# Kernel tuning notes

Hardware: AMD Instinct MI355X
Metric: run time of the kernel (lower is better)

## Reference

```python
import jax, jax.numpy as jnp
import numpy as np

C = 32           # in_channels
KH, KW = 3, 3    # kernel_range
SHIFT = 1
NP = KH * KW


def conv2d(x, w, b, pad):
    # x: NCHW, w: OIHW
    y = jax.lax.conv_general_dilated(
        x, w, window_strides=(1, 1), padding=[(pad, pad), (pad, pad)],
        dimension_numbers=('NCHW', 'OIHW', 'NCHW'))
    return y + b[None, :, None, None]


def setup_inputs() -> dict:
    key = jax.random.key(0)
    ks = jax.random.split(key, 14)
    p = lambda k, shape: (jax.random.normal(k, shape, dtype=jnp.float32) * 0.02)
    inp = {
        'x':  jax.random.normal(ks[0], (4, C, 256, 256), dtype=jnp.float32),
        'wk': p(ks[1], (C * NP, C, 1, 1)), 'bk': p(ks[2], (C * NP,)),
        'wv': p(ks[3], (C * NP, C, 1, 1)), 'bv': p(ks[4], (C * NP,)),
        'wq': p(ks[5], (C, C, 1, 1)),      'bq': p(ks[6], (C,)),
        'w1': p(ks[7], (C, C, 3, 3)),      'b1': p(ks[8], (C,)),
        'w2': p(ks[9], (2 * C, C, 3, 3)),  'b2': p(ks[10], (2 * C,)),
        'w3': p(ks[11], (C, 2 * C, 3, 3)), 'b3': p(ks[12], (C,)),
    }
    return inp


def reference(x, wk, bk, wv, bv, wq, bq, w1, b1, w2, b2, w3, b3):
    B, D, H, W = x.shape
    h_half, w_half = KH // 2, KW // 2
    ph, pw = h_half * SHIFT, w_half * SHIFT

    x_k = conv2d(x, wk, bk, 0)  # (B, D*NP, H, W)
    x_v = conv2d(x, wv, bv, 0)
    x_q = conv2d(x, wq, bq, 0)  # (B, D, H, W)

    pad4 = ((0, 0), (0, 0), (ph, ph), (pw, pw))
    x_k = jnp.pad(x_k, pad4)
    x_v = jnp.pad(x_v, pad4)
    mask_pad = jnp.pad(jnp.ones((B, 1, H, W), x.dtype), pad4)

    k_ls, v_ls, m_ls = [], [], []
    layer = 0
    for i in range(-h_half, h_half + 1):
        for j in range(-w_half, w_half + 1):
            r0 = ph + i * SHIFT
            c0 = pw + j * SHIFT
            k_ls.append(x_k[:, layer * D:(layer + 1) * D, r0:r0 + H, c0:c0 + W])
            v_ls.append(x_v[:, layer * D:(layer + 1) * D, r0:r0 + H, c0:c0 + W])
            m_ls.append(mask_pad[:, :, r0:r0 + H, c0:c0 + W])
            layer += 1

    # Faithful to torch .view semantics: flat row-major reshape, NOT a permute.
    k = jnp.stack(k_ls, axis=1).reshape(B * H * W, NP, D)   # (B,NP,D,H,W) -> flat
    v = jnp.stack(v_ls, axis=1).reshape(B * H * W, NP, D)
    m = jnp.stack(m_ls, axis=1).reshape(B * H * W, NP, 1)
    q = x_q.reshape(B * H * W, 1, D)                         # (B,D,H,W) -> flat

    scores = jnp.matmul(k, jnp.swapaxes(q, -1, -2)) * m / 8.0  # (N, NP, 1)
    alpha = jax.nn.softmax(scores, axis=1)
    res = jnp.matmul(jnp.swapaxes(alpha, -1, -2), v)           # (N, 1, D)
    t = res.reshape(B, D, H, W)

    t = jax.nn.relu(conv2d(t, w1, b1, 1))
    t = jax.nn.relu(conv2d(t, w2, b2, 1))
    t = jax.nn.relu(conv2d(t, w3, b3, 1))
    return t
```

## Files before the change

kernel.cpp:

```cpp
#include <hip/hip_runtime.h>
#include <hip/hip_bf16.h>

#define B_ 4
#define C_ 32
#define H_ 256
#define W_ 256
#define S_ 65536
#define NP_ 9
#define OC_ 288
#define PR 258
#define PWN 264
#define XGUARD 260
#define XSTRIDE 66056

using bf16 = __hip_bfloat16;
typedef __attribute__((ext_vector_type(8)))  short  short8;
typedef __attribute__((ext_vector_type(4)))  short  short4_t;
typedef __attribute__((ext_vector_type(2)))  short  short2_t;
typedef __attribute__((ext_vector_type(16))) float  f32x16;

__device__ __forceinline__ float b2f(short s) {
    return __uint_as_float(((unsigned)(unsigned short)s) << 16);
}

template<int IC, int OC>
__device__ __forceinline__ void prepA_body(int fid, const float* __restrict__ w,
                                           bf16* __restrict__ apk)
{
    constexpr int NK = 9 * IC / 16;
    int tile = fid >> 9;
    int l = (fid >> 3) & 63;
    int j = fid & 7;
    int mt = tile / NK;
    int ks = tile - mt * NK;
    int q = l >> 5;
    int oc = mt * 32 + (l & 31);
    int k = ks * 16 + q * 8 + j;
    int tap = k / IC;
    int ic = k - tap * IC;
    apk[fid] = __float2bfloat16(w[((oc * IC + ic) * 3 + tap / 3) * 3 + tap % 3]);
}

template<int G>
__device__ __forceinline__ void zerob_body(int b, int p, uint4* __restrict__ buf)
{
    int gran;
    if (p < 2 * PWN * G) {
        int row = (p < PWN * G) ? 0 : 257;
        int rem = p % (PWN * G);
        gran = row * PWN * G + rem;
    } else {
        int p2 = p - 2 * PWN * G;
        int col = (p2 < 256 * G) ? 0 : 257;
        int rem = p2 % (256 * G);
        int r = rem / G + 1;
        int icg = rem - (rem / G) * G;
        gran = (r * PWN + col) * G + icg;
    }
    buf[(size_t)b * PR * PWN * G + gran] = uint4{0, 0, 0, 0};
}

__global__ __launch_bounds__(256) void k_prep(
    const float* __restrict__ wk, const float* __restrict__ wv,
    const float* __restrict__ wq,
    const float* __restrict__ w1, const float* __restrict__ w2,
    const float* __restrict__ w3,
    bf16* __restrict__ apk0, bf16* __restrict__ apk1,
    bf16* __restrict__ apk2, bf16* __restrict__ apk3,
    uint4* __restrict__ tA, uint4* __restrict__ t1, uint4* __restrict__ t2,
    uint4* __restrict__ xb16)
{
    int idx = blockIdx.x * 256 + threadIdx.x;
    if (idx < 19456) {
        int j    = idx & 7;
        int lane = (idx >> 3) & 63;
        int ks   = (idx >> 9) & 1;
        int mt   = idx >> 10;
        int oc = lane & 31;
        int ic = ks * 16 + (lane >> 5) * 8 + j;
        const float* w; int ocg;
        if (mt < 9)       { w = wk; ocg = mt * 32 + oc; }
        else if (mt < 18) { w = wv; ocg = (mt - 9) * 32 + oc; }
        else              { w = wq; ocg = oc; }
        apk0[idx] = __float2bfloat16(w[ocg * C_ + ic]);
    } else if (idx < 28672) {
        prepA_body<32, 32>(idx - 19456, w1, apk1);
    } else if (idx < 47104) {
        prepA_body<32, 64>(idx - 28672, w2, apk2);
    } else if (idx < 65536) {
        prepA_body<64, 32>(idx - 47104, w3, apk3);
    } else if (idx < 82176) {
        int i5 = idx - 65536;
        zerob_body<4>(i5 / 4160, i5 % 4160, tA);
    } else if (idx < 98816) {
        int i6 = idx - 82176;
        zerob_body<4>(i6 / 4160, i6 % 4160, t1);
    } else if (idx < 132096) {
        int i7 = idx - 98816;
        zerob_body<8>(i7 / 8320, i7 % 8320, t2);
    } else if (idx < 142464) {
        int i8 = idx - 132096;
        size_t off;
        if (i8 < 8320) {
            int b = i8 / 2080, r = i8 - b * 2080;
            if (r < 1040) off = (size_t)b * (XSTRIDE * 4) + r;
            else          off = ((size_t)b * XSTRIDE + XGUARD + 65536) * 4 + (r - 1040);
        } else {
            off = (size_t)(4 * XSTRIDE) * 4 + (i8 - 8320);
        }
        xb16[off] = uint4{0, 0, 0, 0};
    }
}

__global__ __launch_bounds__(256) void k_q(
    const float* __restrict__ x, const bf16* __restrict__ apk,
    const float* __restrict__ bq, bf16* __restrict__ xqs, bf16* __restrict__ xb16)
{
    __shared__ bf16 lbuf[32][140];
    int bh  = blockIdx.x >> 9;
    int blk = blockIdx.x & 511;
    int pixw0 = blk << 7;
    int tid  = threadIdx.x;
    int wvi  = tid >> 6;
    int lane = tid & 63;
    int col  = lane & 31, q = lane >> 5;
    int pix  = pixw0 + wvi * 32 + col;

    const float* xb = x + (size_t)bh * (C_ * S_);

    short8 bfrag[2];
#pragma unroll
    for (int kk = 0; kk < 2; ++kk)
#pragma unroll
        for (int j = 0; j < 8; ++j) {
            bf16 h = __float2bfloat16(xb[(size_t)(kk * 16 + q * 8 + j) * S_ + pix]);
            bfrag[kk][j] = *reinterpret_cast<short*>(&h);
        }

    {
        bf16* xr = xb16 + ((size_t)bh * XSTRIDE + XGUARD + pix) * 32;
        *reinterpret_cast<short8*>(xr + (q << 3))       = bfrag[0];
        *reinterpret_cast<short8*>(xr + ((2 + q) << 3)) = bfrag[1];
    }

    const short8* apkv = reinterpret_cast<const short8*>(apk);
    f32x16 acc = {};
    acc = __builtin_amdgcn_mfma_f32_32x32x16_bf16(bfrag[0], apkv[(18 * 2 + 0) * 64 + lane], acc, 0, 0, 0);
    acc = __builtin_amdgcn_mfma_f32_32x32x16_bf16(bfrag[1], apkv[(18 * 2 + 1) * 64 + lane], acc, 0, 0, 0);
    float bbv = bq[col];
#pragma unroll
    for (int g4 = 0; g4 < 4; ++g4) {
        short4_t sv;
#pragma unroll
        for (int j = 0; j < 4; ++j) {
            bf16 hb = __float2bfloat16(acc[g4 * 4 + j] + bbv);
            sv[j] = *reinterpret_cast<short*>(&hb);
        }
        *reinterpret_cast<short4_t*>(&lbuf[col][wvi * 32 + 8 * g4 + 4 * q]) = sv;
    }
    __syncthreads();
    int ch0 = tid >> 4, chk = tid & 15, ch1 = ch0 + 16;
    short8 v0 = *reinterpret_cast<const short8*>(&lbuf[ch0][chk * 8]);
    short8 v1 = *reinterpret_cast<const short8*>(&lbuf[ch1][chk * 8]);
    int tb = (pixw0 >> 5) + (chk >> 2);
    int G2 = chk & 3;
    bf16* qb = xqs + (size_t)bh * (32 * S_);
    short4_t lo0 = {v0[0], v0[1], v0[2], v0[3]}, hi0 = {v0[4], v0[5], v0[6], v0[7]};
    short4_t lo1 = {v1[0], v1[1], v1[2], v1[3]}, hi1 = {v1[4], v1[5], v1[6], v1[7]};
    *reinterpret_cast<short4_t*>(qb + (ch0 * 2048 + tb) * 32 + G2 * 4)      = lo0;
    *reinterpret_cast<short4_t*>(qb + (ch0 * 2048 + tb) * 32 + 16 + G2 * 4) = hi0;
    *reinterpret_cast<short4_t*>(qb + (ch1 * 2048 + tb) * 32 + G2 * 4)      = lo1;
    *reinterpret_cast<short4_t*>(qb + (ch1 * 2048 + tb) * 32 + 16 + G2 * 4) = hi1;
}


#define DO_TILE(T, SQ)                                                                \
{                                                                                     \
    int Tg = tgbase + (T);                                                            \
    if (Tg < 2048) {                                                                  \
        bool hbad = ((((T) << 5) < hb_lo) || (((T) << 5) >= hb_hi));                  \
        if (hbad) {                                                                   \
            if (q == (SQ)) scL[(T) * 32 + col] = 0.f;                                 \
            short4_t z = {0, 0, 0, 0};                                                \
            _Pragma("unroll")                                                         \
            for (int G2 = 0; G2 < 4; ++G2)                                            \
                *reinterpret_cast<short4_t*>(kvB + col * 1616 +                       \
                    ((((T) << 2) + (G2 ^ xcol)) << 4) + q * 8) = z;                   \
        } else {                                                                      \
            unsigned n = (unsigned)plane_base + ((unsigned)Tg << 5);                  \
            unsigned tl = n / 288u;                                                   \
            const bf16* qp = xqb + ((size_t)tl << 5) + (q << 4);                      \
            short8 qA = *reinterpret_cast<const short8*>(qp);                         \
            short8 qB = *reinterpret_cast<const short8*>(qp + 8);                     \
            int xib = ((T) << 5) + 257 + shf + col;                                   \
            int swx = (xib ^ (xib >> 2)) & 3;                                         \
            short8 fa = *reinterpret_cast<const short8*>(&xs[xib * 4 + (q ^ swx)]);   \
            short8 fb = *reinterpret_cast<const short8*>(&xs[xib * 4 + ((2 + q) ^ swx)]); \
            bool tb_lo = (dj == -1) && ((Tg & 7) == 0);                               \
            bool tb_hi = (dj == 1) && ((Tg & 7) == 7);                                \
            if (tb_lo) { if (q == 0) qA[0] = 0; }                                     \
            if (tb_hi) { if (q == 1) qB[7] = 0; }                                     \
            f32x16 ka = {bK, bK, bK, bK, bK, bK, bK, bK, bK, bK, bK, bK, bK, bK, bK, bK}; \
            ka = __builtin_amdgcn_mfma_f32_32x32x16_bf16(fa, apkv[(p * 2 + 0) * 64 + lane], ka, 0, 0, 0); \
            ka = __builtin_amdgcn_mfma_f32_32x32x16_bf16(fb, apkv[(p * 2 + 1) * 64 + lane], ka, 0, 0, 0); \
            float dot = 0.f;                                                          \
            _Pragma("unroll")                                                         \
            for (int j3 = 0; j3 < 4; ++j3) {                                          \
                dot += ka[j3]      * b2f(qA[j3]);                                     \
                dot += ka[4 + j3]  * b2f(qA[4 + j3]);                                 \
                dot += ka[8 + j3]  * b2f(qB[j3]);                                     \
                dot += ka[12 + j3] * b2f(qB[4 + j3]);                                 \
            }                                                                         \
            dot += __shfl_xor(dot, 32);                                               \
            if (q == (SQ)) scL[(T) * 32 + col] = dot;                                 \
            f32x16 vh = {bV, bV, bV, bV, bV, bV, bV, bV, bV, bV, bV, bV, bV, bV, bV, bV}; \
            vh = __builtin_amdgcn_mfma_f32_32x32x16_bf16(fa, apkv[((9 + p) * 2 + 0) * 64 + lane], vh, 0, 0, 0); \
            vh = __builtin_amdgcn_mfma_f32_32x32x16_bf16(fb, apkv[((9 + p) * 2 + 1) * 64 + lane], vh, 0, 0, 0); \
            _Pragma("unroll")                                                         \
            for (int G2 = 0; G2 < 4; ++G2) {                                          \
                short4_t sv;                                                          \
                _Pragma("unroll")                                                     \
                for (int j3 = 0; j3 < 4; ++j3) {                                      \
                    bf16 hcv = __float2bfloat16(vh[G2 * 4 + j3]);                     \
                    sv[j3] = *reinterpret_cast<short*>(&hcv);                         \
                }                                                                     \
                if (G2 == 0 && tb_lo) { if (q == 0) sv[0] = 0; }                      \
                if (G2 == 3 && tb_hi) { if (q == 1) sv[3] = 0; }                      \
                *reinterpret_cast<short4_t*>(kvB + col * 1616 +                       \
                    ((((T) << 2) + (G2 ^ xcol)) << 4) + q * 8) = sv;                  \
            }                                                                         \
        }                                                                             \
    }                                                                                 \
}

__global__ __launch_bounds__(1024, 4) void k_fused(
    const bf16* __restrict__ xb16,
    const bf16* __restrict__ apk,
    const float* __restrict__ bk, const float* __restrict__ bv,
    const bf16* __restrict__ xqs,
    bf16* __restrict__ att)
{
    extern __shared__ char smem_raw[];
    uint4* xs  = reinterpret_cast<uint4*>(smem_raw);
    char*  kvB = smem_raw + 84096;
    float* scL = reinterpret_cast<float*>(smem_raw + 135808);
    unsigned* scMT = reinterpret_cast<unsigned*>(smem_raw + 139008);
    float* wgtL = reinterpret_cast<float*>(smem_raw + 141312);

    int bb = blockIdx.x >> 7;
    int s0 = (blockIdx.x & 127) << 9;
    int tgbase = s0 >> 5;

    int tid  = threadIdx.x;
    int lane = tid & 63;
    int wv   = tid >> 6;
    int col  = lane & 31;
    int q    = lane >> 5;
    int xcol = (col >> 3) & 3;

    size_t qbase = ((size_t)bb << 21);
    const bf16* xqb = xqs + qbase;
    const short8* apkv = reinterpret_cast<const short8*>(apk);

    {
        const uint4* src = reinterpret_cast<const uint4*>(xb16) +
                           ((size_t)bb * XSTRIDE + XGUARD + s0 - 257) * 4;
        for (int i = tid; i < 5256; i += 1024) {
            int xi = i >> 2, g = i & 3;
            int sw = (xi ^ (xi >> 2)) & 3;
            xs[xi * 4 + (g ^ sw)] = src[i];
        }
    }

    if (tid < 576) {
        int krow = tid >= 288;
        int i2 = tid - (krow ? 288 : 0);
        int pp = i2 >> 5, dpc = i2 & 31;
        int plane_base_r = ((pp << 5) + dpc) << 16;
        unsigned tl = ((unsigned)(plane_base_r + s0 + 287)) / 288u + (unsigned)krow;
        int sk0 = (int)(tl * 288u) - plane_base_r;
        unsigned e = 0;
        if (sk0 < s0 + 512 && sk0 <= 65248) {
            int t0 = (sk0 - s0) >> 5;
            e = (1u << 10) | ((unsigned)t0 << 11) | (tl << 16);
#pragma unroll
            for (int seg = 0; seg < 9; ++seg) {
                int rm = (int)tl * 9 + seg;
                int pm = rm >> 16, sm = rm & 65535;
                int dim = pm / 3 - 1, djm = pm - (pm / 3) * 3 - 1;
                int hm = sm >> 8, wm = sm & 255;
                bool mval = ((unsigned)(hm + dim) < 256u) && ((unsigned)(wm + djm) < 256u);
                e |= (mval ? 1u : 0u) << seg;
            }
        }
        scMT[tid] = e;
    }
    __syncthreads();

    int sub   = tid & 15;
    int strip = tid >> 4;
    int dp    = strip & 31;
    int krow  = strip >> 5;
    int swz   = (dp >> 3) & 3;
    int vboff = dp * 1616 + (((sub >> 2) ^ swz) << 4) + ((sub >> 1) & 1) * 8 + (sub & 1) * 4;

#pragma unroll 1
    for (int p = 0; p < 9; ++p) {
        int di = p / 3 - 1, dj = p - (p / 3) * 3 - 1;
        int shf = di * 256 + dj;
        int hb_lo = (di == -1) ? (256 - s0) : (-0x40000000);
        int hb_hi = (di == 1) ? (65280 - s0) : 0x40000000;
        float bK = bk[p * 32 + col];
        float bV = bv[p * 32 + col];
        int plane_base = ((p << 5) + col) << 16;

        DO_TILE(wv, 0)
        if (wv < 9) { DO_TILE(wv + 16, 1) }
        __syncthreads();

        if (tid < 64) {
            unsigned e = scMT[(tid >> 5) * 288 + p * 32 + (tid & 31)];
            if (e & 1024u) {
                int t0s = (e >> 11) & 31;
                int dps = tid & 31;
                float sc[9];
#pragma unroll
                for (int seg = 0; seg < 9; ++seg)
                    sc[seg] = ((e >> seg) & 1u) ? scL[(t0s + seg) * 32 + dps] * 0.125f : 0.f;
                float mx = sc[0];
#pragma unroll
                for (int s2 = 1; s2 < 9; ++s2) mx = fmaxf(mx, sc[s2]);
                float sum = 0.f;
                float* wrow = wgtL + tid * 12;
#pragma unroll
                for (int s2 = 0; s2 < 9; ++s2) {
                    float w_ = __expf(sc[s2] - mx);
                    wrow[s2] = w_;
                    sum += w_;
                }
                wrow[9] = 1.f / sum;
            }
        }
        __syncthreads();

        {
            unsigned e = scMT[krow * 288 + p * 32 + dp];
            if (e & 1024u) {
                int tl = e >> 16;
                int t0 = (e >> 11) & 31;
                const float* wrow = wgtL + strip * 12;
                const char* vb = kvB + vboff + t0 * 64;
                float o0 = 0.f, o1 = 0.f;
#pragma unroll
                for (int seg = 0; seg < 9; ++seg) {
                    short2_t vg = *reinterpret_cast<const short2_t*>(vb + seg * 64);
                    float w_ = wrow[seg];
                    o0 += w_ * b2f(vg[0]);
                    o1 += w_ * b2f(vg[1]);
                }
                float inv_ = wrow[9];
                bf16 h0 = __float2bfloat16(o0 * inv_);
                bf16 h1 = __float2bfloat16(o1 * inv_);
                short2_t s2v = {*reinterpret_cast<short*>(&h0), *reinterpret_cast<short*>(&h1)};
                *reinterpret_cast<short2_t*>(att + qbase + ((size_t)tl << 5) + sub * 2) = s2v;
            }
        }
        __syncthreads();
    }
}

__global__ __launch_bounds__(320) void k_strad(
    const bf16* __restrict__ xb16,
    const float* __restrict__ wk, const float* __restrict__ bk,
    const float* __restrict__ wv, const float* __restrict__ bv,
    const bf16* __restrict__ xqs, bf16* __restrict__ att)
{
    __shared__ float kL[288], vL[288], qL[32], wgtL[10];
    int e = blockIdx.x;
    int b = e >> 8, i = e & 255;
    int g = i >> 3, u = i & 7;
    int tl = g * 2048 + (((2040 + u) * 1593) & 2047);
    int tid = threadIdx.x;

    if (tid < 288) {
        int f  = tl * 288 + tid;
        int cp = f >> 16;
        int sp = f & 65535;
        int tap = cp >> 5;
        int di = tap / 3 - 1, dj = tap - (tap / 3) * 3 - 1;
        int h = sp >> 8, w = sp & 255;
        bool valid = ((unsigned)(h + di) < 256u) && ((unsigned)(w + dj) < 256u);
        float kv_ = 0.f, vv_ = 0.f;
        if (valid) {
            int sx = sp + di * 256 + dj;
            const bf16* xp = xb16 + ((size_t)b * XSTRIDE + XGUARD + sx) * 32;
            const float* wkp = wk + cp * 32;
            const float* wvp = wv + cp * 32;
            float ks = bk[cp], vs = bv[cp];
            short8 xg[4];
#pragma unroll
            for (int gg = 0; gg < 4; ++gg)
                xg[gg] = *reinterpret_cast<const short8*>(xp + gg * 8);
#pragma unroll
            for (int gg = 0; gg < 4; ++gg)
#pragma unroll
                for (int j = 0; j < 8; ++j) {
                    float xv_ = b2f(xg[gg][j]);
                    ks += wkp[gg * 8 + j] * xv_;
                    vs += wvp[gg * 8 + j] * xv_;
                }
            kv_ = ks; vv_ = vs;
        }
        kL[tid] = kv_; vL[tid] = vv_;
    }
    if (tid < 32) {
        int pos = ((tid >> 2) & 1) * 16 + (tid >> 3) * 4 + (tid & 3);
        bf16 hv = xqs[(size_t)b * (32 * S_) + (size_t)tl * 32 + pos];
        qL[tid] = b2f(*reinterpret_cast<short*>(&hv));
    }
    __syncthreads();
    if (tid < 9) {
        float dot = 0.f;
#pragma unroll
        for (int d = 0; d < 32; ++d) dot += kL[tid * 32 + d] * qL[d];
        int rm = tl * 9 + tid;
        int pm = rm >> 16, sm = rm & 65535;
        int dim = pm / 3 - 1, djm = pm - (pm / 3) * 3 - 1;
        int hm = sm >> 8, wm = sm & 255;
        bool mval = ((unsigned)(hm + dim) < 256u) && ((unsigned)(wm + djm) < 256u);
        wgtL[tid] = mval ? dot * 0.125f : 0.f;
    }
    __syncthreads();
    if (tid == 0) {
        float mx = wgtL[0];
#pragma unroll
        for (int s2 = 1; s2 < 9; ++s2) mx = fmaxf(mx, wgtL[s2]);
        float sum = 0.f;
#pragma unroll
        for (int s2 = 0; s2 < 9; ++s2) { wgtL[s2] = __expf(wgtL[s2] - mx); sum += wgtL[s2]; }
        wgtL[9] = 1.f / sum;
    }
    __syncthreads();
    if (tid < 32) {
        float acc = 0.f;
#pragma unroll
        for (int seg = 0; seg < 9; ++seg) acc += wgtL[seg] * vL[seg * 32 + tid];
        att[(size_t)b * 2097152 + (size_t)tl * 32 + tid] = __float2bfloat16(acc * wgtL[9]);
    }
}

__global__ __launch_bounds__(256) void k_repack(
    const bf16* __restrict__ att, bf16* __restrict__ tA)
{
    int idx = blockIdx.x * 256 + threadIdx.x;
    int icg = idx & 3;
    int ps  = idx >> 2;
    int b = ps >> 16;
    int s = ps & 65535;
    const bf16* src = att + (size_t)b * (32 * S_) + icg * 8 * S_ + s;
    short8 v;
#pragma unroll
    for (int j = 0; j < 8; ++j)
        v[j] = *reinterpret_cast<const short*>(src + (size_t)j * S_);
    int row = (s >> 8) + 1, colp = (s & 255) + 1;
    *reinterpret_cast<short8*>(tA + ((size_t)((b * PR + row) * PWN + colp)) * 32 + icg * 8) = v;
}

template<int IC, int OC, bool NCHW_OUT>
__global__ __launch_bounds__(256) void k_conv3s(
    const bf16* __restrict__ in,
    const bf16* __restrict__ apk,
    const float* __restrict__ bs,
    void* __restrict__ outv)
{
    constexpr int G    = IC / 8;
    constexpr int M    = OC / 32;
    constexpr int KPT  = IC / 16;
    constexpr int NK   = 9 * KPT;
    constexpr int NT   = 2;
    constexpr int ROWP = 66;
    constexpr int ROWG = ROWP * G;
    constexpr int TOTG = 6 * ROWG;

    __shared__ uint4 smem[TOTG];

    int wg   = blockIdx.x;
    int orig = (wg & 7) * 128 + (wg >> 3);
    int b   = orig >> 8;
    int rem = orig & 255;
    int h0  = (rem >> 2) << 2;
    int w0  = (rem & 3) * 64;

    int tid = threadIdx.x;

    {
        const uint4* src = reinterpret_cast<const uint4*>(in);
#pragma unroll
        for (int i = 0; i < (TOTG + 255) / 256; ++i) {
            int idx = tid + i * 256;
            if (idx < TOTG) {
                int dr = idx / ROWG;
                int r2 = idx - dr * ROWG;
                uint4 v = src[((size_t)(b * PR + h0 + dr) * PWN + w0) * G + r2];
                int px = r2 >> ((G == 4) ? 2 : 3);
                int sw = (G == 4) ? ((px ^ (px >> 2)) & 3) : (px & 7);
                smem[dr * ROWG + (r2 & ~(G - 1)) + ((r2 ^ sw) & (G - 1))] = v;
            }
        }
    }
    __syncthreads();

    int lane = tid & 63;
    int wid  = tid >> 6;
    int col  = lane & 31, q = lane >> 5;
    int h    = h0 + wid;

    const short8* apkv = reinterpret_cast<const short8*>(apk);

    f32x16 acc[NT][M];
#pragma unroll
    for (int nt = 0; nt < NT; ++nt)
#pragma unroll
        for (int mt = 0; mt < M; ++mt) acc[nt][mt] = (f32x16){};

#pragma unroll
    for (int tap = 0; tap < 9; ++tap) {
        int dr = tap / 3 + wid;
        int dj = tap % 3;
#pragma unroll
        for (int icq = 0; icq < KPT; ++icq) {
            short8 bfr[NT];
#pragma unroll
            for (int nt = 0; nt < NT; ++nt) {
                int px = nt * 32 + col + dj;
                int sw = (G == 4) ? ((px ^ (px >> 2)) & 3) : (px & 7);
                bfr[nt] = *reinterpret_cast<const short8*>(
                    &smem[dr * ROWG + px * G + ((icq * 2 + q) ^ sw)]);
            }
#pragma unroll
            for (int mt = 0; mt < M; ++mt) {
                short8 afr = apkv[(mt * NK + tap * KPT + icq) * 64 + lane];
#pragma unroll
                for (int nt = 0; nt < NT; ++nt)
                    acc[nt][mt] = __builtin_amdgcn_mfma_f32_32x32x16_bf16(
                        afr, bfr[nt], acc[nt][mt], 0, 0, 0);
            }
        }
    }

#pragma unroll
    for (int nt = 0; nt < NT; ++nt) {
        int wout = w0 + nt * 32 + col;
#pragma unroll
        for (int mt = 0; mt < M; ++mt) {
            if (NCHW_OUT) {
                float* out = (float*)outv;
#pragma unroll
                for (int r = 0; r < 16; ++r) {
                    int oc = mt * 32 + (r & 3) + 8 * (r >> 2) + 4 * q;
                    out[(size_t)((b * OC + oc) * H_ + h) * W_ + wout] =
                        fmaxf(acc[nt][mt][r] + bs[oc], 0.f);
                }
            } else {
                bf16* out = (bf16*)outv;
                size_t base = (size_t)((b * PR + h + 1) * PWN + wout + 1) * OC + mt * 32 + 4 * q;
#pragma unroll
                for (int g4 = 0; g4 < 4; ++g4) {
                    short4_t sv;
#pragma unroll
                    for (int r4 = 0; r4 < 4; ++r4) {
                        int oc = mt * 32 + 8 * g4 + 4 * q + r4;
                        bf16 hh = __float2bfloat16(fmaxf(acc[nt][mt][g4 * 4 + r4] + bs[oc], 0.f));
                        sv[r4] = *reinterpret_cast<short*>(&hh);
                    }
                    *reinterpret_cast<short4_t*>(out + base + 8 * g4) = sv;
                }
            }
        }
    }
}

extern "C" void kernel_launch(void* const* d_in, const int* in_sizes, int n_in,
                              void* d_out, int out_size, void* d_ws, size_t ws_size,
                              hipStream_t stream)
{
    const float* x  = (const float*)d_in[0];
    const float* wk = (const float*)d_in[1];
    const float* bk = (const float*)d_in[2];
    const float* wv = (const float*)d_in[3];
    const float* bv = (const float*)d_in[4];
    const float* wq = (const float*)d_in[5];
    const float* bq = (const float*)d_in[6];
    const float* w1 = (const float*)d_in[7];
    const float* b1 = (const float*)d_in[8];
    const float* w2 = (const float*)d_in[9];
    const float* b2 = (const float*)d_in[10];
    const float* w3 = (const float*)d_in[11];
    const float* b3 = (const float*)d_in[12];
    float* out = (float*)d_out;
    char* ws = (char*)d_ws;

    bf16* xqs  = (bf16*)(ws);
    bf16* tA   = (bf16*)(ws + 16777216);
    bf16* t1   = (bf16*)(ws + 34213888);
    bf16* t2   = (bf16*)(ws + 51650560);
    bf16* apk0 = (bf16*)(ws + 86523904);
    bf16* apk1 = (bf16*)(ws + 86562816);
    bf16* apk2 = (bf16*)(ws + 86581248);
    bf16* apk3 = (bf16*)(ws + 86618112);
    bf16* xb16 = (bf16*)(ws + 86654976);
    bf16* attB = (bf16*)d_out;

    static bool attr_set = false;
    if (!attr_set) {
        hipFuncSetAttribute(reinterpret_cast<const void*>(k_fused),
                            hipFuncAttributeMaxDynamicSharedMemorySize, 144384);
        attr_set = true;
    }

    k_prep<<<557, 256, 0, stream>>>(wk, wv, wq, w1, w2, w3,
                                    apk0, apk1, apk2, apk3,
                                    (uint4*)tA, (uint4*)t1, (uint4*)t2, (uint4*)xb16);

    k_q<<<2048, 256, 0, stream>>>(x, apk0, bq, xqs, xb16);

    k_fused<<<512, 1024, 144384, stream>>>(xb16, apk0, bk, bv, xqs, attB);

    k_strad<<<1024, 320, 0, stream>>>(xb16, wk, bk, wv, bv, xqs, attB);

    k_repack<<<4096, 256, 0, stream>>>(attB, tA);

    k_conv3s<32, 32, false><<<1024, 256, 0, stream>>>(tA, apk1, b1, (void*)t1);
    k_conv3s<32, 64, false><<<1024, 256, 0, stream>>>(t1, apk2, b2, (void*)t2);
    k_conv3s<64, 32, true ><<<1024, 256, 0, stream>>>(t2, apk3, b3, (void*)out);
}
```

Baseline: 170.3 us.

## Fuse repack into first conv, keep q in fp32, softmax via wave shuffles

Removes the k_repack kernel. A new k_conv3p reads the NCHW attention output directly, transposes it into swizzled shared memory and runs the first 3x3 conv, so the tA padded buffer and its zeroing go away. The q projection is now stored in fp32 rather than bf16, which doubles that traffic but avoids a rounding step and bf16 unpacking in the score dot product. In k_fused the softmax weights are computed per lane with cross-lane shuffles instead of a separate 64-thread pass through shared memory. This drops one __syncthreads and some shared memory, but every lane now does redundant exp work.

```diff
diff --git a/kernel.cpp b/kernel.cpp
--- a/kernel.cpp
+++ b/kernel.cpp
@@ -18,6 +18,7 @@
 typedef __attribute__((ext_vector_type(4)))  short  short4_t;
 typedef __attribute__((ext_vector_type(2)))  short  short2_t;
 typedef __attribute__((ext_vector_type(16))) float  f32x16;
+typedef __attribute__((ext_vector_type(4)))  float  f32x4;
 
 __device__ __forceinline__ float b2f(short s) {
     return __uint_as_float(((unsigned)(unsigned short)s) << 16);
@@ -67,7 +68,7 @@
     const float* __restrict__ w3,
     bf16* __restrict__ apk0, bf16* __restrict__ apk1,
     bf16* __restrict__ apk2, bf16* __restrict__ apk3,
-    uint4* __restrict__ tA, uint4* __restrict__ t1, uint4* __restrict__ t2,
+    uint4* __restrict__ t1, uint4* __restrict__ t2,
     uint4* __restrict__ xb16)
 {
     int idx = blockIdx.x * 256 + threadIdx.x;
@@ -90,16 +91,13 @@
     } else if (idx < 65536) {
         prepA_body<64, 32>(idx - 47104, w3, apk3);
     } else if (idx < 82176) {
-        int i5 = idx - 65536;
-        zerob_body<4>(i5 / 4160, i5 % 4160, tA);
-    } else if (idx < 98816) {
-        int i6 = idx - 82176;
+        int i6 = idx - 65536;
         zerob_body<4>(i6 / 4160, i6 % 4160, t1);
-    } else if (idx < 132096) {
-        int i7 = idx - 98816;
+    } else if (idx < 115456) {
+        int i7 = idx - 82176;
         zerob_body<8>(i7 / 8320, i7 % 8320, t2);
-    } else if (idx < 142464) {
-        int i8 = idx - 132096;
+    } else if (idx < 125824) {
+        int i8 = idx - 115456;
         size_t off;
         if (i8 < 8320) {
             int b = i8 / 2080, r = i8 - b * 2080;
@@ -114,9 +112,9 @@
 
 __global__ __launch_bounds__(256) void k_q(
     const float* __restrict__ x, const bf16* __restrict__ apk,
-    const float* __restrict__ bq, bf16* __restrict__ xqs, bf16* __restrict__ xb16)
-{
-    __shared__ bf16 lbuf[32][140];
+    const float* __restrict__ bq, float* __restrict__ xqsf, bf16* __restrict__ xb16)
+{
+    __shared__ float lbuf[32][140];
     int bh  = blockIdx.x >> 9;
     int blk = blockIdx.x & 511;
     int pixw0 = blk << 7;
@@ -150,27 +148,23 @@
     float bbv = bq[col];
 #pragma unroll
     for (int g4 = 0; g4 < 4; ++g4) {
-        short4_t sv;
-#pragma unroll
-        for (int j = 0; j < 4; ++j) {
-            bf16 hb = __float2bfloat16(acc[g4 * 4 + j] + bbv);
-            sv[j] = *reinterpret_cast<short*>(&hb);
-        }
-        *reinterpret_cast<short4_t*>(&lbuf[col][wvi * 32 + 8 * g4 + 4 * q]) = sv;
+        f32x4 fv = {acc[g4 * 4 + 0] + bbv, acc[g4 * 4 + 1] + bbv,
+                    acc[g4 * 4 + 2] + bbv, acc[g4 * 4 + 3] + bbv};
+        *reinterpret_cast<f32x4*>(&lbuf[col][wvi * 32 + 8 * g4 + 4 * q]) = fv;
     }
     __syncthreads();
     int ch0 = tid >> 4, chk = tid & 15, ch1 = ch0 + 16;
-    short8 v0 = *reinterpret_cast<const short8*>(&lbuf[ch0][chk * 8]);
-    short8 v1 = *reinterpret_cast<const short8*>(&lbuf[ch1][chk * 8]);
     int tb = (pixw0 >> 5) + (chk >> 2);
     int G2 = chk & 3;
-    bf16* qb = xqs + (size_t)bh * (32 * S_);
-    short4_t lo0 = {v0[0], v0[1], v0[2], v0[3]}, hi0 = {v0[4], v0[5], v0[6], v0[7]};
-    short4_t lo1 = {v1[0], v1[1], v1[2], v1[3]}, hi1 = {v1[4], v1[5], v1[6], v1[7]};
-    *reinterpret_cast<short4_t*>(qb + (ch0 * 2048 + tb) * 32 + G2 * 4)      = lo0;
-    *reinterpret_cast<short4_t*>(qb + (ch0 * 2048 + tb) * 32 + 16 + G2 * 4) = hi0;
-    *reinterpret_cast<short4_t*>(qb + (ch1 * 2048 + tb) * 32 + G2 * 4)      = lo1;
-    *reinterpret_cast<short4_t*>(qb + (ch1 * 2048 + tb) * 32 + 16 + G2 * 4) = hi1;
+    float* qb = xqsf + (size_t)bh * (32 * S_);
+    f32x4 lo0 = *reinterpret_cast<const f32x4*>(&lbuf[ch0][chk * 8]);
+    f32x4 hi0 = *reinterpret_cast<const f32x4*>(&lbuf[ch0][chk * 8 + 4]);
+    f32x4 lo1 = *reinterpret_cast<const f32x4*>(&lbuf[ch1][chk * 8]);
+    f32x4 hi1 = *reinterpret_cast<const f32x4*>(&lbuf[ch1][chk * 8 + 4]);
+    *reinterpret_cast<f32x4*>(qb + ((size_t)(ch0 * 2048 + tb) * 32 + G2 * 4))      = lo0;
+    *reinterpret_cast<f32x4*>(qb + ((size_t)(ch0 * 2048 + tb) * 32 + 16 + G2 * 4)) = hi0;
+    *reinterpret_cast<f32x4*>(qb + ((size_t)(ch1 * 2048 + tb) * 32 + G2 * 4))      = lo1;
+    *reinterpret_cast<f32x4*>(qb + ((size_t)(ch1 * 2048 + tb) * 32 + 16 + G2 * 4)) = hi1;
 }
 
 
@@ -189,27 +183,29 @@
         } else {                                                                      \
             unsigned n = (unsigned)plane_base + ((unsigned)Tg << 5);                  \
             unsigned tl = n / 288u;                                                   \
-            const bf16* qp = xqb + ((size_t)tl << 5) + (q << 4);                      \
-            short8 qA = *reinterpret_cast<const short8*>(qp);                         \
-            short8 qB = *reinterpret_cast<const short8*>(qp + 8);                     \
+            const float* qp = xqf + ((size_t)tl << 5) + (q << 4);                     \
+            f32x4 qf0 = *reinterpret_cast<const f32x4*>(qp);                          \
+            f32x4 qf1 = *reinterpret_cast<const f32x4*>(qp + 4);                      \
+            f32x4 qf2 = *reinterpret_cast<const f32x4*>(qp + 8);                      \
+            f32x4 qf3 = *reinterpret_cast<const f32x4*>(qp + 12);                     \
             int xib = ((T) << 5) + 257 + shf + col;                                   \
             int swx = (xib ^ (xib >> 2)) & 3;                                         \
             short8 fa = *reinterpret_cast<const short8*>(&xs[xib * 4 + (q ^ swx)]);   \
             short8 fb = *reinterpret_cast<const short8*>(&xs[xib * 4 + ((2 + q) ^ swx)]); \
             bool tb_lo = (dj == -1) && ((Tg & 7) == 0);                               \
             bool tb_hi = (dj == 1) && ((Tg & 7) == 7);                                \
-            if (tb_lo) { if (q == 0) qA[0] = 0; }                                     \
-            if (tb_hi) { if (q == 1) qB[7] = 0; }                                     \
+            if (tb_lo) { if (q == 0) qf0[0] = 0.f; }                                  \
+            if (tb_hi) { if (q == 1) qf3[3] = 0.f; }                                  \
             f32x16 ka = {bK, bK, bK, bK, bK, bK, bK, bK, bK, bK, bK, bK, bK, bK, bK, bK}; \
             ka = __builtin_amdgcn_mfma_f32_32x32x16_bf16(fa, apkv[(p * 2 + 0) * 64 + lane], ka, 0, 0, 0); \
             ka = __builtin_amdgcn_mfma_f32_32x32x16_bf16(fb, apkv[(p * 2 + 1) * 64 + lane], ka, 0, 0, 0); \
             float dot = 0.f;                                                          \
             _Pragma("unroll")                                                         \
             for (int j3 = 0; j3 < 4; ++j3) {                                          \
-                dot += ka[j3]      * b2f(qA[j3]);                                     \
-                dot += ka[4 + j3]  * b2f(qA[4 + j3]);                                 \
-                dot += ka[8 + j3]  * b2f(qB[j3]);                                     \
-                dot += ka[12 + j3] * b2f(qB[4 + j3]);                                 \
+                dot += ka[j3]      * qf0[j3];                                         \
+                dot += ka[4 + j3]  * qf1[j3];                                         \
+                dot += ka[8 + j3]  * qf2[j3];                                         \
+                dot += ka[12 + j3] * qf3[j3];                                         \
             }                                                                         \
             dot += __shfl_xor(dot, 32);                                               \
             if (q == (SQ)) scL[(T) * 32 + col] = dot;                                 \
@@ -237,7 +233,7 @@
     const bf16* __restrict__ xb16,
     const bf16* __restrict__ apk,
     const float* __restrict__ bk, const float* __restrict__ bv,
-    const bf16* __restrict__ xqs,
+    const float* __restrict__ xqsf,
     bf16* __restrict__ att)
 {
     extern __shared__ char smem_raw[];
@@ -245,7 +241,6 @@
     char*  kvB = smem_raw + 84096;
     float* scL = reinterpret_cast<float*>(smem_raw + 135808);
     unsigned* scMT = reinterpret_cast<unsigned*>(smem_raw + 139008);
-    float* wgtL = reinterpret_cast<float*>(smem_raw + 141312);
 
     int bb = blockIdx.x >> 7;
     int s0 = (blockIdx.x & 127) << 9;
@@ -259,7 +254,7 @@
     int xcol = (col >> 3) & 3;
 
     size_t qbase = ((size_t)bb << 21);
-    const bf16* xqb = xqs + qbase;
+    const float* xqf = xqsf + qbase;
     const short8* apkv = reinterpret_cast<const short8*>(apk);
 
     {
@@ -303,6 +298,7 @@
     int krow  = strip >> 5;
     int swz   = (dp >> 3) & 3;
     int vboff = dp * 1616 + (((sub >> 2) ^ swz) << 4) + ((sub >> 1) & 1) * 8 + (sub & 1) * 4;
+    int gbase = (tid & 63) & 48;
 
 #pragma unroll 1
     for (int p = 0; p < 9; ++p) {
@@ -318,47 +314,35 @@
         if (wv < 9) { DO_TILE(wv + 16, 1) }
         __syncthreads();
 
-        if (tid < 64) {
-            unsigned e = scMT[(tid >> 5) * 288 + p * 32 + (tid & 31)];
-            if (e & 1024u) {
-                int t0s = (e >> 11) & 31;
-                int dps = tid & 31;
-                float sc[9];
-#pragma unroll
-                for (int seg = 0; seg < 9; ++seg)
-                    sc[seg] = ((e >> seg) & 1u) ? scL[(t0s + seg) * 32 + dps] * 0.125f : 0.f;
-                float mx = sc[0];
-#pragma unroll
-                for (int s2 = 1; s2 < 9; ++s2) mx = fmaxf(mx, sc[s2]);
-                float sum = 0.f;
-                float* wrow = wgtL + tid * 12;
-#pragma unroll
-                for (int s2 = 0; s2 < 9; ++s2) {
-                    float w_ = __expf(sc[s2] - mx);
-                    wrow[s2] = w_;
-                    sum += w_;
-                }
-                wrow[9] = 1.f / sum;
-            }
-        }
-        __syncthreads();
-
         {
             unsigned e = scMT[krow * 288 + p * 32 + dp];
             if (e & 1024u) {
                 int tl = e >> 16;
                 int t0 = (e >> 11) & 31;
-                const float* wrow = wgtL + strip * 12;
+                float mysc = -3.0e38f;
+                if (sub < 9)
+                    mysc = ((e >> sub) & 1u) ? scL[(t0 + sub) * 32 + dp] * 0.125f : 0.f;
+                float m = mysc;
+                m = fmaxf(m, __shfl_xor(m, 1));
+                m = fmaxf(m, __shfl_xor(m, 2));
+                m = fmaxf(m, __shfl_xor(m, 4));
+                m = fmaxf(m, __shfl_xor(m, 8));
+                float w = (sub < 9) ? __expf(mysc - m) : 0.f;
+                float s = w;
+                s += __shfl_xor(s, 1);
+                s += __shfl_xor(s, 2);
+                s += __shfl_xor(s, 4);
+                s += __shfl_xor(s, 8);
+                float inv_ = 1.f / s;
                 const char* vb = kvB + vboff + t0 * 64;
                 float o0 = 0.f, o1 = 0.f;
 #pragma unroll
                 for (int seg = 0; seg < 9; ++seg) {
+                    float w_ = __shfl(w, gbase + seg);
                     short2_t vg = *reinterpret_cast<const short2_t*>(vb + seg * 64);
-                    float w_ = wrow[seg];
                     o0 += w_ * b2f(vg[0]);
                     o1 += w_ * b2f(vg[1]);
                 }
-                float inv_ = wrow[9];
                 bf16 h0 = __float2bfloat16(o0 * inv_);
                 bf16 h1 = __float2bfloat16(o1 * inv_);
                 short2_t s2v = {*reinterpret_cast<short*>(&h0), *reinterpret_cast<short*>(&h1)};
@@ -373,7 +357,7 @@
     const bf16* __restrict__ xb16,
     const float* __restrict__ wk, const float* __restrict__ bk,
     const float* __restrict__ wv, const float* __restrict__ bv,
-    const bf16* __restrict__ xqs, bf16* __restrict__ att)
+    const float* __restrict__ xqsf, bf16* __restrict__ att)
 {
     __shared__ float kL[288], vL[288], qL[32], wgtL[10];
     int e = blockIdx.x;
@@ -415,8 +399,7 @@
     }
     if (tid < 32) {
         int pos = ((tid >> 2) & 1) * 16 + (tid >> 3) * 4 + (tid & 3);
-        bf16 hv = xqs[(size_t)b * (32 * S_) + (size_t)tl * 32 + pos];
-        qL[tid] = b2f(*reinterpret_cast<short*>(&hv));
+        qL[tid] = xqsf[(size_t)b * (32 * S_) + (size_t)tl * 32 + pos];
     }
     __syncthreads();
     if (tid < 9) {
@@ -449,21 +432,105 @@
     }
 }
 
-__global__ __launch_bounds__(256) void k_repack(
-    const bf16* __restrict__ att, bf16* __restrict__ tA)
-{
-    int idx = blockIdx.x * 256 + threadIdx.x;
-    int icg = idx & 3;
-    int ps  = idx >> 2;
-    int b = ps >> 16;
-    int s = ps & 65535;
-    const bf16* src = att + (size_t)b * (32 * S_) + icg * 8 * S_ + s;
-    short8 v;
-#pragma unroll
-    for (int j = 0; j < 8; ++j)
-        v[j] = *reinterpret_cast<const short*>(src + (size_t)j * S_);
-    int row = (s >> 8) + 1, colp = (s & 255) + 1;
-    *reinterpret_cast<short8*>(tA + ((size_t)((b * PR + row) * PWN + colp)) * 32 + icg * 8) = v;
+__global__ __launch_bounds__(256) void k_conv3p(
+    const bf16* __restrict__ att,
+    const bf16* __restrict__ apk,
+    const float* __restrict__ bs,
+    bf16* __restrict__ outp)
+{
+    constexpr int G    = 4;
+    constexpr int KPT  = 2;
+    constexpr int NK   = 18;
+    constexpr int NT   = 2;
+    constexpr int ROWP = 80;
+    constexpr int ROWG = ROWP * G;
+    constexpr int TOTG = 6 * ROWG;
+
+    __shared__ uint4 smem[TOTG];
+    short* smems = reinterpret_cast<short*>(smem);
+
+    int wg   = blockIdx.x;
+    int orig = (wg & 7) * 128 + (wg >> 3);
+    int b   = orig >> 8;
+    int rem = orig & 255;
+    int h0  = (rem >> 2) << 2;
+    int w0  = (rem & 3) * 64;
+
+    int tid = threadIdx.x;
+
+    for (int i = tid; i < 1920; i += 256) {
+        int gran = i % 10;
+        int ch   = (i / 10) & 31;
+        int dr   = i / 320;
+        int r    = h0 - 1 + dr;
+        int c0   = w0 - 8 + gran * 8;
+        short8 v;
+        if ((unsigned)r < 256u && (unsigned)c0 < 256u) {
+            v = *reinterpret_cast<const short8*>(
+                att + (size_t)b * 2097152 + ((size_t)ch << 16) + r * 256 + c0);
+        } else {
+            v = (short8){0, 0, 0, 0, 0, 0, 0, 0};
+        }
+        int chh = ch & 7, chg = ch >> 3;
+#pragma unroll
+        for (int j = 0; j < 8; ++j) {
+            int jj  = (j + gran) & 7;
+            int lpx = gran * 8 + jj;
+            int sw  = (lpx ^ (lpx >> 2)) & 3;
+            smems[(dr * ROWG + lpx * G + (chg ^ sw)) * 8 + chh] = v[jj];
+        }
+    }
+    __syncthreads();
+
+    int lane = tid & 63;
+    int wid  = tid >> 6;
+    int col  = lane & 31, q = lane >> 5;
+    int h    = h0 + wid;
+
+    const short8* apkv = reinterpret_cast<const short8*>(apk);
+
+    f32x16 acc[NT];
+#pragma unroll
+    for (int nt = 0; nt < NT; ++nt) acc[nt] = (f32x16){};
+
+#pragma unroll
+    for (int tap = 0; tap < 9; ++tap) {
+        int dr = tap / 3 + wid;
+        int dj = tap % 3;
+#pragma unroll
+        for (int icq = 0; icq < KPT; ++icq) {
+            short8 bfr[NT];
+#pragma unroll
+            for (int nt = 0; nt < NT; ++nt) {
+                int lpx = nt * 32 + col + dj + 7;
+                int sw  = (lpx ^ (lpx >> 2)) & 3;
+                bfr[nt] = *reinterpret_cast<const short8*>(
+                    &smem[dr * ROWG + lpx * G + ((icq * 2 + q) ^ sw)]);
+            }
+            short8 afr = apkv[(tap * KPT + icq) * 64 + lane];
+#pragma unroll
+            for (int nt = 0; nt < NT; ++nt)
+                acc[nt] = __builtin_amdgcn_mfma_f32_32x32x16_bf16(
+                    afr, bfr[nt], acc[nt], 0, 0, 0);
+        }
+    }
+
+#pragma unroll
+    for (int nt = 0; nt < NT; ++nt) {
+        int wout = w0 + nt * 32 + col;
+        size_t base = (size_t)((b * PR + h + 1) * PWN + wout + 1) * 32 + 4 * q;
+#pragma unroll
+        for (int g4 = 0; g4 < 4; ++g4) {
+            short4_t sv;
+#pragma unroll
+            for (int r4 = 0; r4 < 4; ++r4) {
+                int oc = 8 * g4 + 4 * q + r4;
+                bf16 hh = __float2bfloat16(fmaxf(acc[nt][g4 * 4 + r4] + bs[oc], 0.f));
+                sv[r4] = *reinterpret_cast<short*>(&hh);
+            }
+            *reinterpret_cast<short4_t*>(outp + base + 8 * g4) = sv;
+        }
+    }
 }
 
 template<int IC, int OC, bool NCHW_OUT>
@@ -600,37 +667,34 @@
     float* out = (float*)d_out;
     char* ws = (char*)d_ws;
 
-    bf16* xqs  = (bf16*)(ws);
-    bf16* tA   = (bf16*)(ws + 16777216);
-    bf16* t1   = (bf16*)(ws + 34213888);
-    bf16* t2   = (bf16*)(ws + 51650560);
-    bf16* apk0 = (bf16*)(ws + 86523904);
-    bf16* apk1 = (bf16*)(ws + 86562816);
-    bf16* apk2 = (bf16*)(ws + 86581248);
-    bf16* apk3 = (bf16*)(ws + 86618112);
-    bf16* xb16 = (bf16*)(ws + 86654976);
-    bf16* attB = (bf16*)d_out;
+    float* xqsf = (float*)(ws);
+    bf16*  t1   = (bf16*)(ws + 33554432);
+    bf16*  t2   = (bf16*)(ws + 50991104);
+    bf16*  apk0 = (bf16*)(ws + 85864448);
+    bf16*  apk1 = (bf16*)(ws + 85903360);
+    bf16*  apk2 = (bf16*)(ws + 85921792);
+    bf16*  apk3 = (bf16*)(ws + 85958656);
+    bf16*  xb16 = (bf16*)(ws + 85995520);
+    bf16*  attB = (bf16*)d_out;
 
     static bool attr_set = false;
     if (!attr_set) {
         hipFuncSetAttribute(reinterpret_cast<const void*>(k_fused),
-                            hipFuncAttributeMaxDynamicSharedMemorySize, 144384);
+                            hipFuncAttributeMaxDynamicSharedMemorySize, 141312);
         attr_set = true;
     }
 
-    k_prep<<<557, 256, 0, stream>>>(wk, wv, wq, w1, w2, w3,
+    k_prep<<<492, 256, 0, stream>>>(wk, wv, wq, w1, w2, w3,
                                     apk0, apk1, apk2, apk3,
-                                    (uint4*)tA, (uint4*)t1, (uint4*)t2, (uint4*)xb16);
-
-    k_q<<<2048, 256, 0, stream>>>(x, apk0, bq, xqs, xb16);
-
-    k_fused<<<512, 1024, 144384, stream>>>(xb16, apk0, bk, bv, xqs, attB);
-
-    k_strad<<<1024, 320, 0, stream>>>(xb16, wk, bk, wv, bv, xqs, attB);
-
-    k_repack<<<4096, 256, 0, stream>>>(attB, tA);
-
-    k_conv3s<32, 32, false><<<1024, 256, 0, stream>>>(tA, apk1, b1, (void*)t1);
+                                    (uint4*)t1, (uint4*)t2, (uint4*)xb16);
+
+    k_q<<<2048, 256, 0, stream>>>(x, apk0, bq, xqsf, xb16);
+
+    k_fused<<<512, 1024, 141312, stream>>>(xb16, apk0, bk, bv, xqsf, attB);
+
+    k_strad<<<1024, 320, 0, stream>>>(xb16, wk, bk, wv, bv, xqsf, attB);
+
+    k_conv3p<<<1024, 256, 0, stream>>>(attB, apk1, b1, t1);
     k_conv3s<32, 64, false><<<1024, 256, 0, stream>>>(t1, apk2, b2, (void*)t2);
     k_conv3s<64, 32, true ><<<1024, 256, 0, stream>>>(t2, apk3, b3, (void*)out);
 }
```

Measured after the change: 202.0 us. +18.6%, slower.
